# Performance work log

Measured on AMD Instinct MI355X. Metric: run time of the kernel, lower is better.

Reference implementation:

```python
import jax, jax.numpy as jnp
import numpy as np

B, T, N, FI, FO = 4, 8, 1024, 64, 64
ALPHA = 0.2          # LeakyReLU negative slope
NEG_INF = -1e12      # matches torch's -1000000000000.0


def setup_inputs() -> dict:
    key = jax.random.key(0)
    k0, k1, k2, k3, k4 = jax.random.split(key, 5)
    inp = jax.random.normal(k0, (B, T, N, FI), dtype=jnp.float32)
    u = jax.random.uniform(k1, (T, N, N), dtype=jnp.float32)
    adj = jnp.where(u > 0.9, u, 0.0)
    # att_mask: [batch, node, seq] in {0,1}
    att_mask = (jax.random.uniform(k2, (B, N, T)) > 0.2).astype(jnp.float32)
    # xavier-ish init (gain 1.414)
    W = jax.random.normal(k3, (FI, FO), dtype=jnp.float32) * (1.414 * np.sqrt(2.0 / (FI + FO)))
    a = jax.random.normal(k4, (2 * FO, 1), dtype=jnp.float32) * (1.414 * np.sqrt(2.0 / (2 * FO + 1)))
    return {"adj": adj, "inp": inp, "att_mask": att_mask, "W": W, "a": a}


def reference(adj, inp, att_mask, W, a):
    Fo = W.shape[1]
    h = jnp.einsum('btnf,fo->btno', inp, W)               # [B,T,N,Fo]
    # additive decomposition of a^T [h_i || h_j] = a1.h_i + a2.h_j
    a1 = a[:Fo, 0]
    a2 = a[Fo:, 0]
    s1 = jnp.einsum('btno,o->btn', h, a1)                 # contributes along rows (i)
    s2 = jnp.einsum('btno,o->btn', h, a2)                 # contributes along cols (j)
    e = s1[..., :, None] + s2[..., None, :]               # [B,T,N,N]
    e = jnp.where(e > 0, e, ALPHA * e)                    # LeakyReLU
    att = jnp.where(adj > 0, e * adj, NEG_INF)            # adj broadcasts over batch
    att = jax.nn.softmax(att, axis=-1)
    m = jnp.transpose(att_mask, (0, 2, 1))                # [B,T,N]
    att = att * (m[..., :, None] * m[..., None, :])       # outer-product mask
    # dropout is identity in eval mode
    h_prime = jnp.einsum('btij,btjo->btio', att, h)       # [B,T,N,Fo]
    return jax.nn.elu(h_prime)                            # concat=True path
```

## Files before the change

### kernel.cpp

```cpp
#include <hip/hip_runtime.h>
#include <hip/hip_bf16.h>
#include <math.h>

#define N_NODES 1024
#define T_DIM 8

typedef __bf16 bf16x8 __attribute__((ext_vector_type(8)));
typedef float  f32x4  __attribute__((ext_vector_type(4)));

__device__ __forceinline__ float readlane_f(float v, int l) {
    return __uint_as_float(__builtin_amdgcn_readlane(__float_as_uint(v), l));
}

__global__ __launch_bounds__(256) void gat_h_kernel(
    const float* __restrict__ inp, const float* __restrict__ W,
    const float* __restrict__ a, const float* __restrict__ att_mask,
    __bf16* __restrict__ hT, float* __restrict__ s1w, float* __restrict__ s2w)
{
    __shared__ float Wl[64 * 64];
    __shared__ float xl[64 * 64];
    __shared__ __bf16 htl[64 * 66];

    const int tid  = threadIdx.x;
    const int blk  = blockIdx.x;
    const int bt   = blk >> 4;
    const int b    = bt >> 3;
    const int t    = bt & 7;
    const int n0   = (blk & 15) * 64;
    const int lane = tid & 63;
    const int wave = tid >> 6;

    const float4* W4  = (const float4*)W;
    float4*       Wl4 = (float4*)Wl;
    const float4* x4  = (const float4*)(inp + (size_t)(bt * N_NODES + n0) * 64);
    float4*       xl4 = (float4*)xl;
#pragma unroll
    for (int k = 0; k < 4; ++k) {
        Wl4[tid + k * 256] = W4[tid + k * 256];
        xl4[tid + k * 256] = x4[tid + k * 256];
    }
    const float a1 = a[lane];
    const float a2 = a[64 + lane];
    __syncthreads();

#pragma unroll 1
    for (int rg = 0; rg < 16; rg += 4) {
        float xr[4], acc[4];
#pragma unroll
        for (int q = 0; q < 4; ++q) {
            xr[q]  = xl[(wave * 16 + rg + q) * 64 + lane];
            acc[q] = 0.f;
        }
#pragma unroll
        for (int f = 0; f < 64; ++f) {
            float w = Wl[f * 64 + lane];
#pragma unroll
            for (int q = 0; q < 4; ++q)
                acc[q] = fmaf(readlane_f(xr[q], f), w, acc[q]);
        }
#pragma unroll
        for (int q = 0; q < 4; ++q) {
            const int r = wave * 16 + rg + q;
            float v1 = acc[q] * a1, v2 = acc[q] * a2;
#pragma unroll
            for (int off = 32; off; off >>= 1) {
                v1 += __shfl_xor(v1, off, 64);
                v2 += __shfl_xor(v2, off, 64);
            }
            if (lane == 0) {
                s1w[bt * N_NODES + n0 + r] = v1;
                s2w[bt * N_NODES + n0 + r] = v2;
            }
            const float mjr = att_mask[((size_t)b * N_NODES + n0 + r) * T_DIM + t];
            htl[lane * 66 + r] = (__bf16)(acc[q] * mjr);
        }
    }
    __syncthreads();

    {
        const int o  = tid >> 2;
        const int r0 = (tid & 3) * 16;
        unsigned u[8];
#pragma unroll
        for (int k = 0; k < 8; ++k)
            u[k] = *(const unsigned*)&htl[o * 66 + r0 + 2 * k];
        uint4* dst = (uint4*)(hT + (size_t)(bt * 64 + o) * N_NODES + n0 + r0);
        dst[0] = make_uint4(u[0], u[1], u[2], u[3]);
        dst[1] = make_uint4(u[4], u[5], u[6], u[7]);
    }
}

__global__ __launch_bounds__(64) void gat_attn_kernel(
    const float* __restrict__ adj, const float* __restrict__ att_mask,
    const __bf16* __restrict__ hT, const float* __restrict__ s1w,
    const float* __restrict__ s2w, float* __restrict__ out)
{
    const int bt    = blockIdx.y;
    const int b     = bt >> 3;
    const int t     = bt & 7;
    const int irow0 = blockIdx.x * 16;
    const int lane  = threadIdx.x;
    const int l15   = lane & 15;
    const int quad  = lane >> 4;

    f32x4 acc[4];
#pragma unroll
    for (int nc = 0; nc < 4; ++nc) acc[nc] = (f32x4){0.f, 0.f, 0.f, 0.f};
    float lsum = 0.f;
    const float s1r = s1w[bt * N_NODES + irow0 + l15];

    const float*  adjp  = adj + (size_t)t * N_NODES * N_NODES
                              + (size_t)(irow0 + l15) * N_NODES + quad * 8;
    const __bf16* hlane = hT + (size_t)bt * 64 * N_NODES
                             + (size_t)l15 * N_NODES + quad * 8;
    const float*  s2p   = s2w + bt * N_NODES + quad * 8;

    float4 adjc[4], s2c[4];
    bf16x8 hc[8];
#pragma unroll
    for (int k = 0; k < 2; ++k) {
        adjc[k]     = *(const float4*)(adjp + k * 4);
        adjc[2 + k] = *(const float4*)(adjp + 32 + k * 4);
        s2c[k]      = *(const float4*)(s2p + k * 4);
        s2c[2 + k]  = *(const float4*)(s2p + 32 + k * 4);
    }
#pragma unroll
    for (int kc = 0; kc < 2; ++kc)
#pragma unroll
        for (int nc = 0; nc < 4; ++nc)
            hc[kc * 4 + nc] = *(const bf16x8*)(hlane + (size_t)nc * 16 * N_NODES + kc * 32);

#pragma unroll 2
    for (int it = 0; it < 16; ++it) {
        const int j1 = (it < 15) ? (it + 1) * 64 : 0;

        float4 adjn[4], s2n[4];
        bf16x8 hn[8];
#pragma unroll
        for (int k = 0; k < 2; ++k) {
            adjn[k]     = *(const float4*)(adjp + j1 + k * 4);
            adjn[2 + k] = *(const float4*)(adjp + j1 + 32 + k * 4);
            s2n[k]      = *(const float4*)(s2p + j1 + k * 4);
            s2n[2 + k]  = *(const float4*)(s2p + j1 + 32 + k * 4);
        }
#pragma unroll
        for (int kc = 0; kc < 2; ++kc)
#pragma unroll
            for (int nc = 0; nc < 4; ++nc)
                hn[kc * 4 + nc] = *(const bf16x8*)(hlane + (size_t)nc * 16 * N_NODES + j1 + kc * 32);

        const float* ac = (const float*)adjc;
        const float* sc = (const float*)s2c;
        bf16x8 af[2];
#pragma unroll
        for (int kc = 0; kc < 2; ++kc)
#pragma unroll
            for (int m = 0; m < 8; ++m) {
                float av = ac[kc * 8 + m];
                float e  = s1r + sc[kc * 8 + m];
                e = fmaxf(e, 0.2f * e);
                float p = (av > 0.f) ? __expf(e * av) : 0.f;
                lsum += p;
                af[kc][m] = (__bf16)p;
            }

#pragma unroll
        for (int nc = 0; nc < 4; ++nc)
            acc[nc] = __builtin_amdgcn_mfma_f32_16x16x32_bf16(af[0], hc[nc], acc[nc], 0, 0, 0);
#pragma unroll
        for (int nc = 0; nc < 4; ++nc)
            acc[nc] = __builtin_amdgcn_mfma_f32_16x16x32_bf16(af[1], hc[4 + nc], acc[nc], 0, 0, 0);

#pragma unroll
        for (int k = 0; k < 4; ++k) { adjc[k] = adjn[k]; s2c[k] = s2n[k]; }
#pragma unroll
        for (int k = 0; k < 8; ++k) hc[k] = hn[k];
    }

    lsum += __shfl_xor(lsum, 16, 64);
    lsum += __shfl_xor(lsum, 32, 64);

#pragma unroll
    for (int reg = 0; reg < 4; ++reg) {
        const int i = irow0 + quad * 4 + reg;
        float ls = __shfl(lsum, quad * 4 + reg, 64);
        float mi = att_mask[((size_t)b * N_NODES + i) * T_DIM + t];
        float scale = mi / ls;
#pragma unroll
        for (int nc = 0; nc < 4; ++nc) {
            float v = acc[nc][reg] * scale;
            v = (v > 0.f) ? v : (__expf(v) - 1.f);
            out[((size_t)bt * N_NODES + i) * 64 + nc * 16 + l15] = v;
        }
    }
}

extern "C" void kernel_launch(void* const* d_in, const int* in_sizes, int n_in,
                              void* d_out, int out_size, void* d_ws, size_t ws_size,
                              hipStream_t stream) {
    (void)in_sizes; (void)n_in; (void)out_size; (void)ws_size;
    const float* adj      = (const float*)d_in[0];
    const float* inp      = (const float*)d_in[1];
    const float* att_mask = (const float*)d_in[2];
    const float* W        = (const float*)d_in[3];
    const float* a        = (const float*)d_in[4];
    float* out = (float*)d_out;

    __bf16* hT  = (__bf16*)d_ws;
    float*  s1w = (float*)((char*)d_ws + (size_t)4 * 1024 * 1024);
    float*  s2w = s1w + 32 * N_NODES;

    gat_h_kernel<<<512, 256, 0, stream>>>(inp, W, a, att_mask, hT, s1w, s2w);
    dim3 grid(64, 32);
    gat_attn_kernel<<<grid, 64, 0, stream>>>(adj, att_mask, hT, s1w, s2w, out);
}
```

Before: 149.6 us.

## Pre-tile adjacency and h into MFMA fragment layout with staggered j-tile start

Adds a pre-pass kernel that copies adj into a per-16-row, per-64-column tiled layout, so each lane's fragment in the attention kernel is one contiguous 64-byte chunk. The h kernel now writes bf16 h directly in MFMA B-fragment order instead of a transposed row-major layout. The attention kernel starts its j loop at a tile offset that depends on the block index, spreading concurrent blocks across different memory regions. The cost is an extra full pass over adj (32 MB read and 32 MB written) every call, in exchange for fully coalesced loads in the main kernel.

```diff
diff --git a/kernel.cpp b/kernel.cpp
--- a/kernel.cpp
+++ b/kernel.cpp
@@ -12,21 +12,48 @@
     return __uint_as_float(__builtin_amdgcn_readlane(__float_as_uint(v), l));
 }
 
+__global__ __launch_bounds__(256) void adj_tile_kernel(
+    const float* __restrict__ adj, float* __restrict__ adjT)
+{
+    const int t     = blockIdx.y;
+    const int itile = blockIdx.x;
+    const int tid   = threadIdx.x;
+    const int lane  = tid & 63;
+    const int w     = tid >> 6;
+
+    const float* src = adj + (size_t)t * N_NODES * N_NODES
+                           + (size_t)(itile * 16 + (lane & 15)) * N_NODES
+                           + (lane >> 4) * 8;
+    float* dst = adjT + (size_t)(t * 64 + itile) * 16 * 1024 + lane * 16;
+
+#pragma unroll
+    for (int jj = 0; jj < 4; ++jj) {
+        const int jt = w + jj * 4;
+        f32x4 v0 = *(const f32x4*)(src + jt * 64);
+        f32x4 v1 = *(const f32x4*)(src + jt * 64 + 4);
+        f32x4 v2 = *(const f32x4*)(src + jt * 64 + 32);
+        f32x4 v3 = *(const f32x4*)(src + jt * 64 + 36);
+        f32x4* d = (f32x4*)(dst + (size_t)jt * 1024);
+        d[0] = v0; d[1] = v1; d[2] = v2; d[3] = v3;
+    }
+}
+
 __global__ __launch_bounds__(256) void gat_h_kernel(
     const float* __restrict__ inp, const float* __restrict__ W,
     const float* __restrict__ a, const float* __restrict__ att_mask,
-    __bf16* __restrict__ hT, float* __restrict__ s1w, float* __restrict__ s2w)
+    __bf16* __restrict__ hF, float* __restrict__ s1w, float* __restrict__ s2w)
 {
     __shared__ float Wl[64 * 64];
     __shared__ float xl[64 * 64];
-    __shared__ __bf16 htl[64 * 66];
+    __shared__ __bf16 htl[64 * 72];
 
     const int tid  = threadIdx.x;
     const int blk  = blockIdx.x;
     const int bt   = blk >> 4;
     const int b    = bt >> 3;
     const int t    = bt & 7;
-    const int n0   = (blk & 15) * 64;
+    const int nt   = blk & 15;
+    const int n0   = nt * 64;
     const int lane = tid & 63;
     const int wave = tid >> 6;
 
@@ -72,36 +99,41 @@
                 s2w[bt * N_NODES + n0 + r] = v2;
             }
             const float mjr = att_mask[((size_t)b * N_NODES + n0 + r) * T_DIM + t];
-            htl[lane * 66 + r] = (__bf16)(acc[q] * mjr);
+            htl[lane * 72 + r] = (__bf16)(acc[q] * mjr);
         }
     }
     __syncthreads();
 
     {
-        const int o  = tid >> 2;
-        const int r0 = (tid & 3) * 16;
-        unsigned u[8];
-#pragma unroll
-        for (int k = 0; k < 8; ++k)
-            u[k] = *(const unsigned*)&htl[o * 66 + r0 + 2 * k];
-        uint4* dst = (uint4*)(hT + (size_t)(bt * 64 + o) * N_NODES + n0 + r0);
-        dst[0] = make_uint4(u[0], u[1], u[2], u[3]);
-        dst[1] = make_uint4(u[4], u[5], u[6], u[7]);
+        const int l  = tid & 63;
+        const int w  = tid >> 6;
+        __bf16* tbase = hF + (size_t)(bt * 16 + nt) * 4096;
+#pragma unroll
+        for (int cc = 0; cc < 2; ++cc) {
+            const int c  = w + cc * 4;
+            const int nc = c & 3;
+            const int kc = c >> 2;
+            bf16x8 v = *(const bf16x8*)&htl[(nc * 16 + (l & 15)) * 72
+                                            + (l >> 4) * 8 + kc * 32];
+            *(bf16x8*)(tbase + (c * 64 + l) * 8) = v;
+        }
     }
 }
 
 __global__ __launch_bounds__(64) void gat_attn_kernel(
-    const float* __restrict__ adj, const float* __restrict__ att_mask,
-    const __bf16* __restrict__ hT, const float* __restrict__ s1w,
+    const float* __restrict__ adjT, const float* __restrict__ att_mask,
+    const __bf16* __restrict__ hF, const float* __restrict__ s1w,
     const float* __restrict__ s2w, float* __restrict__ out)
 {
     const int bt    = blockIdx.y;
     const int b     = bt >> 3;
     const int t     = bt & 7;
-    const int irow0 = blockIdx.x * 16;
+    const int itile = blockIdx.x;
+    const int irow0 = itile * 16;
     const int lane  = threadIdx.x;
     const int l15   = lane & 15;
     const int quad  = lane >> 4;
+    const int phase = itile & 15;
 
     f32x4 acc[4];
 #pragma unroll
@@ -109,45 +141,47 @@
     float lsum = 0.f;
     const float s1r = s1w[bt * N_NODES + irow0 + l15];
 
-    const float*  adjp  = adj + (size_t)t * N_NODES * N_NODES
-                              + (size_t)(irow0 + l15) * N_NODES + quad * 8;
-    const __bf16* hlane = hT + (size_t)bt * 64 * N_NODES
-                             + (size_t)l15 * N_NODES + quad * 8;
-    const float*  s2p   = s2w + bt * N_NODES + quad * 8;
-
-    float4 adjc[4], s2c[4];
+    const float*  atb = adjT + (size_t)(t * 64 + itile) * 16 * 1024 + lane * 16;
+    const __bf16* htb = hF + (size_t)bt * 16 * 4096 + lane * 8;
+    const float*  s2p = s2w + bt * N_NODES + quad * 8;
+
+    f32x4  adjc[4];
+    f32x4  s2c[4];
     bf16x8 hc[8];
-#pragma unroll
-    for (int k = 0; k < 2; ++k) {
-        adjc[k]     = *(const float4*)(adjp + k * 4);
-        adjc[2 + k] = *(const float4*)(adjp + 32 + k * 4);
-        s2c[k]      = *(const float4*)(s2p + k * 4);
-        s2c[2 + k]  = *(const float4*)(s2p + 32 + k * 4);
-    }
-#pragma unroll
-    for (int kc = 0; kc < 2; ++kc)
-#pragma unroll
-        for (int nc = 0; nc < 4; ++nc)
-            hc[kc * 4 + nc] = *(const bf16x8*)(hlane + (size_t)nc * 16 * N_NODES + kc * 32);
+    {
+        const int jt = phase;
+        const float* ap = atb + (size_t)jt * 1024;
+#pragma unroll
+        for (int k = 0; k < 4; ++k) adjc[k] = *(const f32x4*)(ap + k * 4);
+#pragma unroll
+        for (int k = 0; k < 2; ++k) {
+            s2c[k]     = *(const f32x4*)(s2p + jt * 64 + k * 4);
+            s2c[2 + k] = *(const f32x4*)(s2p + jt * 64 + 32 + k * 4);
+        }
+        const __bf16* hp = htb + (size_t)jt * 4096;
+#pragma unroll
+        for (int c = 0; c < 8; ++c) hc[c] = *(const bf16x8*)(hp + c * 512);
+    }
 
 #pragma unroll 2
     for (int it = 0; it < 16; ++it) {
-        const int j1 = (it < 15) ? (it + 1) * 64 : 0;
-
-        float4 adjn[4], s2n[4];
+        const int jn = (it + 1 + phase) & 15;
+
+        f32x4  adjn[4], s2n[4];
         bf16x8 hn[8];
-#pragma unroll
-        for (int k = 0; k < 2; ++k) {
-            adjn[k]     = *(const float4*)(adjp + j1 + k * 4);
-            adjn[2 + k] = *(const float4*)(adjp + j1 + 32 + k * 4);
-            s2n[k]      = *(const float4*)(s2p + j1 + k * 4);
-            s2n[2 + k]  = *(const float4*)(s2p + j1 + 32 + k * 4);
-        }
-#pragma unroll
-        for (int kc = 0; kc < 2; ++kc)
-#pragma unroll
-            for (int nc = 0; nc < 4; ++nc)
-                hn[kc * 4 + nc] = *(const bf16x8*)(hlane + (size_t)nc * 16 * N_NODES + j1 + kc * 32);
+        {
+            const float* ap = atb + (size_t)jn * 1024;
+#pragma unroll
+            for (int k = 0; k < 4; ++k) adjn[k] = *(const f32x4*)(ap + k * 4);
+#pragma unroll
+            for (int k = 0; k < 2; ++k) {
+                s2n[k]     = *(const f32x4*)(s2p + jn * 64 + k * 4);
+                s2n[2 + k] = *(const f32x4*)(s2p + jn * 64 + 32 + k * 4);
+            }
+            const __bf16* hp = htb + (size_t)jn * 4096;
+#pragma unroll
+            for (int c = 0; c < 8; ++c) hn[c] = *(const bf16x8*)(hp + c * 512);
+        }
 
         const float* ac = (const float*)adjc;
         const float* sc = (const float*)s2c;
@@ -174,7 +208,7 @@
 #pragma unroll
         for (int k = 0; k < 4; ++k) { adjc[k] = adjn[k]; s2c[k] = s2n[k]; }
 #pragma unroll
-        for (int k = 0; k < 8; ++k) hc[k] = hn[k];
+        for (int c = 0; c < 8; ++c) hc[c] = hn[c];
     }
 
     lsum += __shfl_xor(lsum, 16, 64);
@@ -206,11 +240,14 @@
     const float* a        = (const float*)d_in[4];
     float* out = (float*)d_out;
 
-    __bf16* hT  = (__bf16*)d_ws;
-    float*  s1w = (float*)((char*)d_ws + (size_t)4 * 1024 * 1024);
-    float*  s2w = s1w + 32 * N_NODES;
-
-    gat_h_kernel<<<512, 256, 0, stream>>>(inp, W, a, att_mask, hT, s1w, s2w);
+    float*  adjT = (float*)d_ws;
+    __bf16* hF   = (__bf16*)((char*)d_ws + (size_t)32 * 1024 * 1024);
+    float*  s1w  = (float*)((char*)d_ws + (size_t)36 * 1024 * 1024);
+    float*  s2w  = s1w + 32 * N_NODES;
+
+    dim3 gA2(64, 8);
+    adj_tile_kernel<<<gA2, 256, 0, stream>>>(adj, adjT);
+    gat_h_kernel<<<512, 256, 0, stream>>>(inp, W, a, att_mask, hF, s1w, s2w);
     dim3 grid(64, 32);
-    gat_attn_kernel<<<grid, 64, 0, stream>>>(adj, att_mask, hT, s1w, s2w, out);
-}
+    gat_attn_kernel<<<grid, 64, 0, stream>>>(adjT, att_mask, hF, s1w, s2w, out);
+}
```

After: 141.5 us. 1.06x faster.
